# Optimization experiments

Measured on AMD Instinct MI355X. Metric: run time of the kernel, lower is better.

The kernel has to match this reference:

```python
import jax, jax.numpy as jnp
import numpy as np

EMBED = 768
HEADS = 12
HEAD_DIM = EMBED // HEADS
HIDDEN = 4 * EMBED
EPS = 1e-5


def _layernorm(x, g, b):
    mu = jnp.mean(x, axis=-1, keepdims=True)
    var = jnp.var(x, axis=-1, keepdims=True)
    return (x - mu) * jax.lax.rsqrt(var + EPS) * g + b


def setup_inputs() -> dict:
    key = jax.random.key(0)
    ks = jax.random.split(key, 12)
    s_e = 1.0 / np.sqrt(EMBED)
    s_h = 1.0 / np.sqrt(HIDDEN)
    return {
        "x": jax.random.normal(ks[0], (2, 2048, EMBED), dtype=jnp.float32),
        "ln1_g": jnp.ones((EMBED,), jnp.float32),
        "ln1_b": jnp.zeros((EMBED,), jnp.float32),
        "qkv_w": jax.random.uniform(ks[1], (EMBED, 3 * EMBED), jnp.float32, -s_e, s_e),
        "qkv_b": jax.random.uniform(ks[2], (3 * EMBED,), jnp.float32, -s_e, s_e),
        "proj_w": jax.random.uniform(ks[3], (EMBED, EMBED), jnp.float32, -s_e, s_e),
        "proj_b": jax.random.uniform(ks[4], (EMBED,), jnp.float32, -s_e, s_e),
        "ln2_g": jnp.ones((EMBED,), jnp.float32),
        "ln2_b": jnp.zeros((EMBED,), jnp.float32),
        "fc1_w": jax.random.uniform(ks[5], (EMBED, HIDDEN), jnp.float32, -s_e, s_e),
        "fc1_b": jax.random.uniform(ks[6], (HIDDEN,), jnp.float32, -s_e, s_e),
        "fc2_w": jax.random.uniform(ks[7], (HIDDEN, EMBED), jnp.float32, -s_h, s_h),
        "fc2_b": jax.random.uniform(ks[8], (EMBED,), jnp.float32, -s_h, s_h),
    }


def reference(x, ln1_g, ln1_b, qkv_w, qkv_b, proj_w, proj_b,
              ln2_g, ln2_b, fc1_w, fc1_b, fc2_w, fc2_b):
    B, L, C = x.shape
    scale = HEAD_DIM ** -0.5

    # --- attention sublayer (pre-LN) ---
    h = _layernorm(x, ln1_g, ln1_b)
    qkv = h @ qkv_w + qkv_b                       # [B, L, 3C]
    qkv = qkv.reshape(B, L, 3, HEADS, HEAD_DIM)
    q = jnp.transpose(qkv[:, :, 0], (0, 2, 1, 3))  # [B, H, L, D]
    k = jnp.transpose(qkv[:, :, 1], (0, 2, 1, 3))
    v = jnp.transpose(qkv[:, :, 2], (0, 2, 1, 3))
    attn = jnp.einsum('bhqd,bhkd->bhqk', q, k) * scale  # [B, H, L, L]
    attn = jax.nn.softmax(attn, axis=-1)
    out = jnp.einsum('bhqk,bhkd->bhqd', attn, v)  # [B, H, L, D]
    out = jnp.transpose(out, (0, 2, 1, 3)).reshape(B, L, C)
    x = x + (out @ proj_w + proj_b)

    # --- FFN sublayer (pre-LN) ---
    h = _layernorm(x, ln2_g, ln2_b)
    h = jax.nn.gelu(h @ fc1_w + fc1_b, approximate=False)
    x = x + (h @ fc2_w + fc2_b)
    return x
```

## Files before the change

kernel.cpp:

```cpp
#include <hip/hip_runtime.h>
#include <hip/hip_bf16.h>
#include <math.h>

#define EMBED   768
#define NHEADS  12
#define HD      64
#define HIDDEN  3072
#define SEQ     2048
#define BATCH   2
#define ROWS    (BATCH*SEQ)

#define QSCALE  0.1803368801111204f

typedef __bf16 bf16_t;
typedef __attribute__((ext_vector_type(8))) __bf16 bf16x8;
typedef __attribute__((ext_vector_type(4))) __bf16 bf16x4;
typedef __attribute__((ext_vector_type(4))) float f32x4;

static __device__ __forceinline__ f32x4 mfma16(bf16x8 a, bf16x8 b, f32x4 c) {
  return __builtin_amdgcn_mfma_f32_16x16x32_bf16(a, b, c, 0, 0, 0);
}

#if defined(__HIP_DEVICE_COMPILE__) && __has_builtin(__builtin_amdgcn_exp2f)
static __device__ __forceinline__ float fast_exp2(float x) {
  return __builtin_amdgcn_exp2f(x);
}
#else
static __device__ __forceinline__ float fast_exp2(float x) { return exp2f(x); }
#endif

#if defined(__HIP_DEVICE_COMPILE__) && __has_builtin(__builtin_amdgcn_rcpf)
static __device__ __forceinline__ float fast_rcp(float x) {
  return __builtin_amdgcn_rcpf(x);
}
#else
static __device__ __forceinline__ float fast_rcp(float x) { return 1.0f / x; }
#endif

typedef __attribute__((address_space(1))) const void gas_void;
typedef __attribute__((address_space(3))) void las_void;
static __device__ __forceinline__ void gll16(const void* g, void* l) {
  __builtin_amdgcn_global_load_lds((gas_void*)g, (las_void*)l, 16, 0, 0);
}

__global__ __launch_bounds__(256) void prep_kernel(
    const float* __restrict__ w0, bf16_t* __restrict__ o0,
    const float* __restrict__ w1, bf16_t* __restrict__ o1,
    const float* __restrict__ w2, bf16_t* __restrict__ o2,
    const float* __restrict__ w3, bf16_t* __restrict__ o3,
    const float* __restrict__ x,  const float* __restrict__ g,
    const float* __restrict__ bt, bf16_t* __restrict__ lnout)
{
  __shared__ float tile[32][33];
  __shared__ float red[8];
  int lin = blockIdx.x;
  if (lin < 6912) {
    const float* in; bf16_t* out; int R, C, bx, by;
    if (lin < 1728)      { in = w0; out = o0; R = 768;  C = 2304; bx = lin % 72; by = lin / 72; }
    else if (lin < 2304) { in = w1; out = o1; R = 768;  C = 768;  lin -= 1728; bx = lin % 24; by = lin / 24; }
    else if (lin < 4608) { in = w2; out = o2; R = 768;  C = 3072; lin -= 2304; bx = lin % 96; by = lin / 96; }
    else                 { in = w3; out = o3; R = 3072; C = 768;  lin -= 4608; bx = lin % 24; by = lin / 24; }
    int c0 = bx * 32, r0 = by * 32;
    int tx = threadIdx.x & 31, ty = threadIdx.x >> 5;
    #pragma unroll
    for (int p = 0; p < 4; ++p) {
      int r = ty + p * 8;
      tile[r][tx] = in[(size_t)(r0 + r) * C + c0 + tx];
    }
    __syncthreads();
    #pragma unroll
    for (int p = 0; p < 4; ++p) {
      int cc = ty + p * 8;
      out[(size_t)(c0 + cc) * R + r0 + tx] = (bf16_t)tile[tx][cc];
    }
    return;
  }
  int row = lin - 6912;
  int tid = threadIdx.x;
  const float* xr = x + (size_t)row * EMBED;
  float v0 = xr[tid], v1 = xr[tid + 256], v2 = xr[tid + 512];
  float s  = v0 + v1 + v2;
  float s2 = v0*v0 + v1*v1 + v2*v2;
  #pragma unroll
  for (int o = 32; o >= 1; o >>= 1) {
    s  += __shfl_xor(s,  o, 64);
    s2 += __shfl_xor(s2, o, 64);
  }
  int wave = tid >> 6, lane = tid & 63;
  if (lane == 0) { red[wave] = s; red[wave + 4] = s2; }
  __syncthreads();
  s  = red[0] + red[1] + red[2] + red[3];
  s2 = red[4] + red[5] + red[6] + red[7];
  float mu  = s * (1.0f / EMBED);
  float var = s2 * (1.0f / EMBED) - mu * mu;
  float rs  = rsqrtf(var + 1e-5f);
  bf16_t* orow = lnout + (size_t)row * EMBED;
  orow[tid]       = (bf16_t)((v0 - mu) * rs * g[tid]       + bt[tid]);
  orow[tid + 256] = (bf16_t)((v1 - mu) * rs * g[tid + 256] + bt[tid + 256]);
  orow[tid + 512] = (bf16_t)((v2 - mu) * rs * g[tid + 512] + bt[tid + 512]);
}

__global__ __launch_bounds__(256) void ln_kernel(
    const float* __restrict__ x, const float* __restrict__ g,
    const float* __restrict__ bt, bf16_t* __restrict__ out)
{
  int row = blockIdx.x;
  int tid = threadIdx.x;
  const float* xr = x + (size_t)row * EMBED;
  float v0 = xr[tid], v1 = xr[tid + 256], v2 = xr[tid + 512];
  float s  = v0 + v1 + v2;
  float s2 = v0*v0 + v1*v1 + v2*v2;
  #pragma unroll
  for (int o = 32; o >= 1; o >>= 1) {
    s  += __shfl_xor(s,  o, 64);
    s2 += __shfl_xor(s2, o, 64);
  }
  __shared__ float red[8];
  int wave = tid >> 6, lane = tid & 63;
  if (lane == 0) { red[wave] = s; red[wave + 4] = s2; }
  __syncthreads();
  s  = red[0] + red[1] + red[2] + red[3];
  s2 = red[4] + red[5] + red[6] + red[7];
  float mu  = s * (1.0f / EMBED);
  float var = s2 * (1.0f / EMBED) - mu * mu;
  float rs  = rsqrtf(var + 1e-5f);
  bf16_t* orow = out + (size_t)row * EMBED;
  orow[tid]       = (bf16_t)((v0 - mu) * rs * g[tid]       + bt[tid]);
  orow[tid + 256] = (bf16_t)((v1 - mu) * rs * g[tid + 256] + bt[tid + 256]);
  orow[tid + 512] = (bf16_t)((v2 - mu) * rs * g[tid + 512] + bt[tid + 512]);
}

template<int MODE, int BN, int SK = 1>
__global__ __launch_bounds__(256) void gemm_kernel(
    const bf16_t* __restrict__ A, const bf16_t* __restrict__ WT,
    const float* __restrict__ bias, const float* __restrict__ res,
    void* __restrict__ outp, bf16_t* __restrict__ vt, int N, int K)
{
  constexpr int JT = BN / 32;
  __shared__ bf16_t As[2 * 128 * 64];
  __shared__ bf16_t Bs[2 * BN * 64];
  int tid = threadIdx.x;
  int lane = tid & 63, wave = tid >> 6;
  int l15 = lane & 15, quad = lane >> 4;
  int wm = wave >> 1, wn = wave & 1;

  int Nn = N / BN;
  int lin = blockIdx.x;
  int kslice = 0, k_lo = 0, k_hi = K;
  if (MODE == 4) {
    kslice = lin % SK; lin /= SK;
    k_lo = kslice * (K / SK); k_hi = k_lo + K / SK;
  }
  int bm = (lin & 7) + 8 * ((lin >> 3) / Nn);
  int bn = (lin >> 3) % Nn;
  int m0 = bm * 128, n0 = bn * BN;

  f32x4 acc[4][JT];
  #pragma unroll
  for (int i = 0; i < 4; ++i)
    #pragma unroll
    for (int j = 0; j < JT; ++j)
      acc[i][j] = (f32x4){0.f, 0.f, 0.f, 0.f};

  int grow = lane >> 3;
  int gcol = ((lane & 7) ^ grow) * 8;
  const bf16_t* abase = A  + (size_t)(m0 + wave * 32 + grow) * K + gcol;
  const bf16_t* bbase = WT + (size_t)(n0 + wave * (BN / 4) + grow) * K + gcol;
  int swk = l15 & 7;

  auto stageg = [&](int k0, int buf) {
    bf16_t* asp = &As[buf * (128 * 64)];
    bf16_t* bsp = &Bs[buf * (BN * 64)];
    #pragma unroll
    for (int a = 0; a < 4; ++a)
      gll16(abase + (size_t)a * 8 * K + k0, &asp[(wave * 32 + a * 8) * 64]);
    #pragma unroll
    for (int a = 0; a < BN / 32; ++a)
      gll16(bbase + (size_t)a * 8 * K + k0, &bsp[(wave * (BN / 4) + a * 8) * 64]);
  };

  int nsteps = (k_hi - k_lo) / 64;
  stageg(k_lo, 0);

  for (int t = 0; t < nsteps; ++t) {
    if (t + 1 < nsteps) {
      stageg(k_lo + (t + 1) * 64, (t + 1) & 1);
      if constexpr (BN == 128)
        __asm__ volatile("s_waitcnt vmcnt(8)" ::: "memory");
      else
        __asm__ volatile("s_waitcnt vmcnt(6)" ::: "memory");
    } else {
      __asm__ volatile("s_waitcnt vmcnt(0)" ::: "memory");
    }
    __builtin_amdgcn_s_barrier();
    __builtin_amdgcn_sched_barrier(0);

    const bf16_t* asp = &As[(t & 1) * (128 * 64)];
    const bf16_t* bsp = &Bs[(t & 1) * (BN * 64)];
    #pragma unroll
    for (int g = 0; g < 2; ++g) {
      bf16x8 af[4], bfr[JT];
      #pragma unroll
      for (int i = 0; i < 4; ++i)
        af[i] = *(const bf16x8*)
            &asp[(wm * 64 + i * 16 + l15) * 64 + (((g * 4 + quad) ^ swk) * 8)];
      #pragma unroll
      for (int j = 0; j < JT; ++j)
        bfr[j] = *(const bf16x8*)
            &bsp[(wn * (BN / 2) + j * 16 + l15) * 64 + (((g * 4 + quad) ^ swk) * 8)];
      #pragma unroll
      for (int i = 0; i < 4; ++i)
        #pragma unroll
        for (int j = 0; j < JT; ++j)
          acc[i][j] = mfma16(af[i], bfr[j], acc[i][j]);
    }
    __asm__ volatile("s_waitcnt lgkmcnt(0)" ::: "memory");
    __builtin_amdgcn_s_barrier();
  }

  #pragma unroll
  for (int i = 0; i < 4; ++i) {
    int mbase = m0 + wm * 64 + i * 16 + quad * 4;
    #pragma unroll
    for (int j = 0; j < JT; ++j) {
      int n = n0 + wn * (BN / 2) + j * 16 + l15;
      float bn_ = (MODE == 4 && kslice != 0) ? 0.f : bias[n];
      if (MODE == 3 && n >= 1536) {
        int dcol = n - 1536;
        int hh = dcol >> 6, dd = dcol & 63;
        int bsel = mbase >> 11, l = mbase & 2047;
        union { bf16_t b4[4]; uint2 u; } pk;
        #pragma unroll
        for (int r = 0; r < 4; ++r)
          pk.b4[r] = (bf16_t)(acc[i][j][r] + bn_);
        *(uint2*)&vt[(((size_t)bsel * NHEADS + hh) * HD + dd) * SEQ + l] = pk.u;
        continue;
      }
      #pragma unroll
      for (int r = 0; r < 4; ++r) {
        size_t idx = (size_t)(mbase + r) * N + n;
        float v = acc[i][j][r] + bn_;
        if (MODE == 1) {
          float e = fast_exp2(fminf(v * (2.3020807f + 0.10293776f * v * v), 120.f));
          v = v * e * fast_rcp(e + 1.0f);
        }
        if (MODE == 3 && n < 768) v *= QSCALE;
        if (MODE == 2) {
          v += res[idx];
          ((float*)outp)[idx] = v;
        } else if (MODE == 4) {
          atomicAdd((float*)outp + idx, v);
        } else {
          ((bf16_t*)outp)[idx] = (bf16_t)v;
        }
      }
    }
  }
}

__global__ __launch_bounds__(256, 3) void attn_kernel(
    const bf16_t* __restrict__ qkv, const bf16_t* __restrict__ vt,
    bf16_t* __restrict__ attnout)
{
  __attribute__((aligned(16))) __shared__ bf16_t smem[4 * 3 * 2048];
  __shared__ float dsumf[4][64];

  int qt = blockIdx.x, h = blockIdx.y, b = blockIdx.z;
  int tid = threadIdx.x;
  int wave = tid >> 6, lane = tid & 63;
  int l15 = lane & 15, quad = lane >> 4;
  int q0 = qt * 64;
  int bh = b * NHEADS + h;

  bf16_t* wbase = smem + wave * 3 * 2048;

  bf16x8 bq[4][2];
  #pragma unroll
  for (int qi = 0; qi < 4; ++qi) {
    const bf16_t* qrow = qkv + (size_t)(b * SEQ + q0 + qi * 16 + l15) * 2304
                             + h * HD + quad * 8;
    bq[qi][0] = *(const bf16x8*)qrow;
    bq[qi][1] = *(const bf16x8*)(qrow + 32);
  }
  __asm__ volatile("s_waitcnt vmcnt(0)" ::: "memory");

  f32x4 accO[4][4];
  f32x4 accL[4];
  #pragma unroll
  for (int qi = 0; qi < 4; ++qi) {
    accL[qi] = (f32x4){0.f, 0.f, 0.f, 0.f};
    #pragma unroll
    for (int t2 = 0; t2 < 4; ++t2)
      accO[qi][t2] = (f32x4){0.f, 0.f, 0.f, 0.f};
  }

  bf16x8 ones;
  #pragma unroll
  for (int r = 0; r < 8; ++r) ones[r] = (bf16_t)1.0f;

  int krow_l = lane >> 3;
  int kchunk = ((lane & 7) ^ krow_l) * 8;
  const bf16_t* ksrc0 = qkv + (size_t)(b * SEQ + wave * 16 + krow_l) * 2304
                            + 768 + h * HD + kchunk;
  int vrow_l = lane >> 1;
  int vchunk = ((lane & 1) ^ ((vrow_l >> 2) & 1)) * 8;
  const bf16_t* vsrc0 = vt + ((size_t)bh * HD + vrow_l) * SEQ + wave * 16 + vchunk;

  constexpr int NIT = SEQ / 64;

  auto stage = [&](int t) {
    bf16_t* kb = wbase + (t % 3) * 2048;
    bf16_t* vb = kb + 1024;
    const bf16_t* ks = ksrc0 + (size_t)(t * 64) * 2304;
    const bf16_t* vs = vsrc0 + t * 64;
    #pragma unroll
    for (int p = 0; p < 2; ++p) {
      gll16(ks + (size_t)(p * 8) * 2304, kb + p * 512);
      gll16(vs + (size_t)(p * 32) * SEQ, vb + p * 512);
    }
  };

  stage(0);
  stage(1);

  int vphys = (((quad >> 1) ^ ((l15 >> 2) & 1)) * 8) + (quad & 1) * 4;

  for (int p = 0; p < NIT / 2; ++p) {
    int ta = 2 * p, tb = 2 * p + 1;
    __asm__ volatile("s_waitcnt vmcnt(0)" ::: "memory");

    const bf16_t* kba = wbase + (ta % 3) * 2048;
    const bf16_t* vba = kba + 1024;
    const bf16_t* kbb = wbase + (tb % 3) * 2048;
    const bf16_t* vbb = kbb + 1024;

    bf16x8 aka[2], akb[2];
    #pragma unroll
    for (int f = 0; f < 2; ++f) {
      int koff = (((f * 4 + quad) ^ (l15 & 7)) * 8);
      aka[f] = *(const bf16x8*)&kba[l15 * 64 + koff];
      akb[f] = *(const bf16x8*)&kbb[l15 * 64 + koff];
    }

    bf16x8 bv8[4];
    #pragma unroll
    for (int t2 = 0; t2 < 4; ++t2) {
      bf16x4 lo = *(const bf16x4*)&vba[(t2 * 16 + l15) * 16 + vphys];
      bf16x4 hi = *(const bf16x4*)&vbb[(t2 * 16 + l15) * 16 + vphys];
      bf16x8 c;
      #pragma unroll
      for (int r = 0; r < 4; ++r) { c[r] = lo[r]; c[r + 4] = hi[r]; }
      bv8[t2] = c;
    }

    __asm__ volatile("s_waitcnt lgkmcnt(0)" ::: "memory");
    if (p < NIT / 2 - 1) {
      stage(2 * p + 2);
      stage(2 * p + 3);
    }

    #pragma unroll
    for (int qi = 0; qi < 4; ++qi) {
      f32x4 sa = (f32x4){0.f, 0.f, 0.f, 0.f};
      sa = mfma16(aka[0], bq[qi][0], sa);
      sa = mfma16(aka[1], bq[qi][1], sa);
      f32x4 sb = (f32x4){0.f, 0.f, 0.f, 0.f};
      sb = mfma16(akb[0], bq[qi][0], sb);
      sb = mfma16(akb[1], bq[qi][1], sb);
      bf16x8 ap;
      #pragma unroll
      for (int r = 0; r < 4; ++r) {
        ap[r]     = (bf16_t)fast_exp2(sa[r]);
        ap[r + 4] = (bf16_t)fast_exp2(sb[r]);
      }
      accL[qi] = mfma16(ap, ones, accL[qi]);
      #pragma unroll
      for (int t2 = 0; t2 < 4; ++t2)
        accO[qi][t2] = mfma16(ap, bv8[t2], accO[qi][t2]);
    }
  }

  if (l15 == 0) {
    #pragma unroll
    for (int qi = 0; qi < 4; ++qi)
      #pragma unroll
      for (int r = 0; r < 4; ++r)
        dsumf[wave][qi * 16 + quad * 4 + r] = accL[qi][r];
  }
  __syncthreads();

  float* slabf = (float*)smem;

  for (int pass = 0; pass < 2; ++pass) {
    #pragma unroll
    for (int qi2 = 0; qi2 < 2; ++qi2) {
      int qi = pass * 2 + qi2;
      #pragma unroll
      for (int t2 = 0; t2 < 4; ++t2)
        #pragma unroll
        for (int r = 0; r < 4; ++r)
          slabf[wave * 2048 + (qi2 * 16 + quad * 4 + r) * 64 + t2 * 16 + l15]
              = accO[qi][t2][r];
    }
    __syncthreads();
    int row = tid >> 3;
    int d0 = (tid & 7) * 8;
    f32x4 o0 = (f32x4){0.f,0.f,0.f,0.f}, o1 = (f32x4){0.f,0.f,0.f,0.f};
    #pragma unroll
    for (int sw = 0; sw < 4; ++sw) {
      o0 += *(const f32x4*)&slabf[sw * 2048 + row * 64 + d0];
      o1 += *(const f32x4*)&slabf[sw * 2048 + row * 64 + d0 + 4];
    }
    int q_abs = pass * 32 + row;
    float den = dsumf[0][q_abs] + dsumf[1][q_abs] + dsumf[2][q_abs] + dsumf[3][q_abs];
    float inv = 1.0f / den;
    bf16_t ob[8];
    #pragma unroll
    for (int j = 0; j < 4; ++j) {
      ob[j]     = (bf16_t)(o0[j] * inv);
      ob[j + 4] = (bf16_t)(o1[j] * inv);
    }
    *(uint4*)&attnout[(size_t)(b * SEQ + q0 + q_abs) * EMBED + h * HD + d0]
        = *(const uint4*)ob;
    if (pass == 0) __syncthreads();
  }
}

extern "C" void kernel_launch(void* const* d_in, const int* in_sizes, int n_in,
                              void* d_out, int out_size, void* d_ws, size_t ws_size,
                              hipStream_t stream) {
  (void)in_sizes; (void)n_in; (void)out_size; (void)ws_size;
  const float* x      = (const float*)d_in[0];
  const float* ln1_g  = (const float*)d_in[1];
  const float* ln1_b  = (const float*)d_in[2];
  const float* qkv_w  = (const float*)d_in[3];
  const float* qkv_b  = (const float*)d_in[4];
  const float* proj_w = (const float*)d_in[5];
  const float* proj_b = (const float*)d_in[6];
  const float* ln2_g  = (const float*)d_in[7];
  const float* ln2_b  = (const float*)d_in[8];
  const float* fc1_w  = (const float*)d_in[9];
  const float* fc1_b  = (const float*)d_in[10];
  const float* fc2_w  = (const float*)d_in[11];
  const float* fc2_b  = (const float*)d_in[12];
  float* out = (float*)d_out;

  char* p = (char*)d_ws;
  bf16_t* wqkvT  = (bf16_t*)p; p += (size_t)2304 * 768 * 2;
  bf16_t* wprojT = (bf16_t*)p; p += (size_t)768 * 768 * 2;
  bf16_t* wfc1T  = (bf16_t*)p; p += (size_t)3072 * 768 * 2;
  bf16_t* wfc2T  = (bf16_t*)p; p += (size_t)768 * 3072 * 2;
  bf16_t* hbuf   = (bf16_t*)p; p += (size_t)ROWS * 768 * 2;
  bf16_t* qkv    = (bf16_t*)p;
  bf16_t* hid    = (bf16_t*)p; p += (size_t)ROWS * 3072 * 2;
  bf16_t* vt     = (bf16_t*)p; p += (size_t)BATCH * NHEADS * HD * SEQ * 2;
  bf16_t* attno  = (bf16_t*)p; p += (size_t)ROWS * 768 * 2;

  prep_kernel<<<6912 + ROWS, 256, 0, stream>>>(
      qkv_w, wqkvT, proj_w, wprojT, fc1_w, wfc1T, fc2_w, wfc2T,
      x, ln1_g, ln1_b, hbuf);

  gemm_kernel<3,128><<<32 * (2304/128), 256, 0, stream>>>(
      hbuf, wqkvT, qkv_b, nullptr, qkv, vt, 2304, 768);
  attn_kernel<<<dim3(SEQ/64, NHEADS, BATCH), 256, 0, stream>>>(qkv, vt, attno);
  gemm_kernel<2,64><<<32 * (768/64), 256, 0, stream>>>(
      attno, wprojT, proj_b, x, out, nullptr, 768, 768);

  ln_kernel<<<ROWS, 256, 0, stream>>>(out, ln2_g, ln2_b, hbuf);
  gemm_kernel<1,128><<<32 * (3072/128), 256, 0, stream>>>(
      hbuf, wfc1T, fc1_b, nullptr, hid, nullptr, 3072, 768);
  gemm_kernel<4,64,2><<<2 * 32 * (768/64), 256, 0, stream>>>(
      hid, wfc2T, fc2_b, nullptr, out, nullptr, 768, 3072);
}
```

Before: 267.8 us.

## Single-buffer LDS for wide GEMM tiles and remap attention blocks per XCD

GEMMs with BN=128 now use a single LDS buffer and a plain load-sync-compute-sync loop instead of double buffering. This halves their shared memory so more blocks can be resident, at the cost of no longer overlapping global loads with MFMA work. The attention launch becomes a 1D grid of 768 blocks, remapped so each XCD (chosen by blockIdx mod 8) handles three whole batch-head pairs. That keeps K/V for one head in a single XCD's L2.

```diff
diff --git a/kernel.cpp b/kernel.cpp
--- a/kernel.cpp
+++ b/kernel.cpp
@@ -137,8 +137,9 @@
     void* __restrict__ outp, bf16_t* __restrict__ vt, int N, int K)
 {
   constexpr int JT = BN / 32;
-  __shared__ bf16_t As[2 * 128 * 64];
-  __shared__ bf16_t Bs[2 * BN * 64];
+  constexpr int NBUF = (BN == 64) ? 2 : 1;
+  __shared__ bf16_t As[NBUF * 128 * 64];
+  __shared__ bf16_t Bs[NBUF * BN * 64];
   int tid = threadIdx.x;
   int lane = tid & 63, wave = tid >> 6;
   int l15 = lane & 15, quad = lane >> 4;
@@ -168,54 +169,80 @@
   const bf16_t* bbase = WT + (size_t)(n0 + wave * (BN / 4) + grow) * K + gcol;
   int swk = l15 & 7;
 
-  auto stageg = [&](int k0, int buf) {
-    bf16_t* asp = &As[buf * (128 * 64)];
-    bf16_t* bsp = &Bs[buf * (BN * 64)];
-    #pragma unroll
-    for (int a = 0; a < 4; ++a)
-      gll16(abase + (size_t)a * 8 * K + k0, &asp[(wave * 32 + a * 8) * 64]);
-    #pragma unroll
-    for (int a = 0; a < BN / 32; ++a)
-      gll16(bbase + (size_t)a * 8 * K + k0, &bsp[(wave * (BN / 4) + a * 8) * 64]);
-  };
-
-  int nsteps = (k_hi - k_lo) / 64;
-  stageg(k_lo, 0);
-
-  for (int t = 0; t < nsteps; ++t) {
-    if (t + 1 < nsteps) {
-      stageg(k_lo + (t + 1) * 64, (t + 1) & 1);
-      if constexpr (BN == 128)
-        __asm__ volatile("s_waitcnt vmcnt(8)" ::: "memory");
-      else
+  if constexpr (NBUF == 2) {
+    auto stageg = [&](int k0, int buf) {
+      bf16_t* asp = &As[buf * (128 * 64)];
+      bf16_t* bsp = &Bs[buf * (BN * 64)];
+      #pragma unroll
+      for (int a = 0; a < 4; ++a)
+        gll16(abase + (size_t)a * 8 * K + k0, &asp[(wave * 32 + a * 8) * 64]);
+      #pragma unroll
+      for (int a = 0; a < BN / 32; ++a)
+        gll16(bbase + (size_t)a * 8 * K + k0, &bsp[(wave * (BN / 4) + a * 8) * 64]);
+    };
+    int nsteps = (k_hi - k_lo) / 64;
+    stageg(k_lo, 0);
+    for (int t = 0; t < nsteps; ++t) {
+      if (t + 1 < nsteps) {
+        stageg(k_lo + (t + 1) * 64, (t + 1) & 1);
         __asm__ volatile("s_waitcnt vmcnt(6)" ::: "memory");
-    } else {
-      __asm__ volatile("s_waitcnt vmcnt(0)" ::: "memory");
-    }
-    __builtin_amdgcn_s_barrier();
-    __builtin_amdgcn_sched_barrier(0);
-
-    const bf16_t* asp = &As[(t & 1) * (128 * 64)];
-    const bf16_t* bsp = &Bs[(t & 1) * (BN * 64)];
-    #pragma unroll
-    for (int g = 0; g < 2; ++g) {
-      bf16x8 af[4], bfr[JT];
-      #pragma unroll
-      for (int i = 0; i < 4; ++i)
-        af[i] = *(const bf16x8*)
-            &asp[(wm * 64 + i * 16 + l15) * 64 + (((g * 4 + quad) ^ swk) * 8)];
-      #pragma unroll
-      for (int j = 0; j < JT; ++j)
-        bfr[j] = *(const bf16x8*)
-            &bsp[(wn * (BN / 2) + j * 16 + l15) * 64 + (((g * 4 + quad) ^ swk) * 8)];
-      #pragma unroll
-      for (int i = 0; i < 4; ++i)
+      } else {
+        __asm__ volatile("s_waitcnt vmcnt(0)" ::: "memory");
+      }
+      __builtin_amdgcn_s_barrier();
+      __builtin_amdgcn_sched_barrier(0);
+
+      const bf16_t* asp = &As[(t & 1) * (128 * 64)];
+      const bf16_t* bsp = &Bs[(t & 1) * (BN * 64)];
+      #pragma unroll
+      for (int g = 0; g < 2; ++g) {
+        bf16x8 af[4], bfr[JT];
+        #pragma unroll
+        for (int i = 0; i < 4; ++i)
+          af[i] = *(const bf16x8*)
+              &asp[(wm * 64 + i * 16 + l15) * 64 + (((g * 4 + quad) ^ swk) * 8)];
         #pragma unroll
         for (int j = 0; j < JT; ++j)
-          acc[i][j] = mfma16(af[i], bfr[j], acc[i][j]);
-    }
-    __asm__ volatile("s_waitcnt lgkmcnt(0)" ::: "memory");
-    __builtin_amdgcn_s_barrier();
+          bfr[j] = *(const bf16x8*)
+              &bsp[(wn * (BN / 2) + j * 16 + l15) * 64 + (((g * 4 + quad) ^ swk) * 8)];
+        #pragma unroll
+        for (int i = 0; i < 4; ++i)
+          #pragma unroll
+          for (int j = 0; j < JT; ++j)
+            acc[i][j] = mfma16(af[i], bfr[j], acc[i][j]);
+      }
+      __asm__ volatile("s_waitcnt lgkmcnt(0)" ::: "memory");
+      __builtin_amdgcn_s_barrier();
+    }
+  } else {
+    for (int k0 = k_lo; k0 < k_hi; k0 += 64) {
+      #pragma unroll
+      for (int a = 0; a < 4; ++a)
+        gll16(abase + (size_t)a * 8 * K + k0, &As[(wave * 32 + a * 8) * 64]);
+      #pragma unroll
+      for (int a = 0; a < BN / 32; ++a)
+        gll16(bbase + (size_t)a * 8 * K + k0, &Bs[(wave * (BN / 4) + a * 8) * 64]);
+      __syncthreads();
+
+      #pragma unroll
+      for (int g = 0; g < 2; ++g) {
+        bf16x8 af[4], bfr[JT];
+        #pragma unroll
+        for (int i = 0; i < 4; ++i)
+          af[i] = *(const bf16x8*)
+              &As[(wm * 64 + i * 16 + l15) * 64 + (((g * 4 + quad) ^ swk) * 8)];
+        #pragma unroll
+        for (int j = 0; j < JT; ++j)
+          bfr[j] = *(const bf16x8*)
+              &Bs[(wn * (BN / 2) + j * 16 + l15) * 64 + (((g * 4 + quad) ^ swk) * 8)];
+        #pragma unroll
+        for (int i = 0; i < 4; ++i)
+          #pragma unroll
+          for (int j = 0; j < JT; ++j)
+            acc[i][j] = mfma16(af[i], bfr[j], acc[i][j]);
+      }
+      __syncthreads();
+    }
   }
 
   #pragma unroll
@@ -265,12 +292,17 @@
   __attribute__((aligned(16))) __shared__ bf16_t smem[4 * 3 * 2048];
   __shared__ float dsumf[4][64];
 
-  int qt = blockIdx.x, h = blockIdx.y, b = blockIdx.z;
+  int lin = blockIdx.x;
+  int xcd = lin & 7;
+  int idx = lin >> 3;
+  int bh  = xcd * 3 + (idx >> 5);
+  int qt  = idx & 31;
+  int b = bh / NHEADS, h = bh % NHEADS;
+
   int tid = threadIdx.x;
   int wave = tid >> 6, lane = tid & 63;
   int l15 = lane & 15, quad = lane >> 4;
   int q0 = qt * 64;
-  int bh = b * NHEADS + h;
 
   bf16_t* wbase = smem + wave * 3 * 2048;
 
@@ -462,7 +494,7 @@
 
   gemm_kernel<3,128><<<32 * (2304/128), 256, 0, stream>>>(
       hbuf, wqkvT, qkv_b, nullptr, qkv, vt, 2304, 768);
-  attn_kernel<<<dim3(SEQ/64, NHEADS, BATCH), 256, 0, stream>>>(qkv, vt, attno);
+  attn_kernel<<<768, 256, 0, stream>>>(qkv, vt, attno);
   gemm_kernel<2,64><<<32 * (768/64), 256, 0, stream>>>(
       attno, wprojT, proj_b, x, out, nullptr, 768, 768);
 
```

New measurement: 258.9 us. 3.3% less time.
